# Kernel tuning notes

Hardware: AMD Instinct MI355X
Metric: run time of the kernel (lower is better)

## Reference

```python
import jax, jax.numpy as jnp
import numpy as np

B_SZ, D, HW, STRIDE, HEADS, DK, DV = 32, 64, 64, 4, 2, 32, 32
N = HW * HW                      # 4096 query tokens
M = (HW // STRIDE) ** 2          # 256 key/value tokens
EPS = 1e-5


def setup_inputs() -> dict:
    key = jax.random.key(0)
    ks = jax.random.split(key, 8)
    w = lambda k, s: jax.random.normal(k, s, dtype=jnp.float32) * 0.02
    return {
        "x": jax.random.normal(ks[0], (B_SZ, D, HW, HW), dtype=jnp.float32),
        "W_dw": jax.random.normal(ks[1], (D, 1, STRIDE, STRIDE), dtype=jnp.float32) * 0.1,
        "b_dw": jnp.zeros((D,), jnp.float32),
        "Wq": w(ks[2], (HEADS * DK, D)), "bq": jnp.zeros((HEADS * DK,), jnp.float32),
        "Wk": w(ks[3], (HEADS * DK, D)), "bk": jnp.zeros((HEADS * DK,), jnp.float32),
        "Wv": w(ks[4], (HEADS * DV, D)), "bv": jnp.zeros((HEADS * DV,), jnp.float32),
        "Wo": w(ks[5], (D, HEADS * DV)), "bo": jnp.zeros((D,), jnp.float32),
        "B": jax.random.normal(ks[6], (1, HEADS, N, M), dtype=jnp.float32),
    }


def reference(x, W_dw, b_dw, Wq, bq, Wk, bk, Wv, bv, Wo, bo, B):
    b, c, h, w = x.shape
    heads = B.shape[1]
    dk = Wq.shape[0] // heads
    dv = Wv.shape[0] // heads
    s = W_dw.shape[-1]

    # LayerNorm over (C, H, W), no affine params
    mu = jnp.mean(x, axis=(1, 2, 3), keepdims=True)
    var = jnp.mean((x - mu) ** 2, axis=(1, 2, 3), keepdims=True)
    xn = (x - mu) * jax.lax.rsqrt(var + EPS)

    # Q from normalized input: (b, N, c)
    xr = jnp.transpose(xn.reshape(b, c, h * w), (0, 2, 1))
    q = (xr @ Wq.T + bq).reshape(b, h * w, heads, dk).transpose(0, 2, 1, 3)

    # K/V from depthwise-conv downsample of the *unnormalized* x (as in source)
    kc = jax.lax.conv_general_dilated(
        x, W_dw, window_strides=(s, s), padding="VALID",
        feature_group_count=c,
        dimension_numbers=("NCHW", "OIHW", "NCHW"),
    ) + b_dw[None, :, None, None]
    kh, kw = kc.shape[2], kc.shape[3]
    kv_in = jnp.transpose(kc.reshape(b, c, kh * kw), (0, 2, 1))  # (b, M, c)
    k = (kv_in @ Wk.T + bk).reshape(b, kh * kw, heads, dk).transpose(0, 2, 1, 3)
    v = (kv_in @ Wv.T + bv).reshape(b, kh * kw, heads, dv).transpose(0, 2, 1, 3)

    # Attention with additive relative bias
    attn = jnp.einsum("bhid,bhjd->bhij", q, k) * (dk ** -0.5) + B
    attn = jax.nn.softmax(attn, axis=-1)
    tmp = jnp.einsum("bhij,bhjd->bhid", attn, v)           # (b, heads, N, dv)
    tmp = tmp.transpose(0, 2, 1, 3).reshape(b, h * w, heads * dv)

    # Output proj; NOTE: source does a raw .view(b, d, h, w) (reshape, not permute)
    out = (tmp @ Wo.T + bo).reshape(b, c, h, w)
    return out + x
```

## Files before the change

### kernel.cpp

```cpp
#include <hip/hip_runtime.h>

typedef float f32x4 __attribute__((ext_vector_type(4)));

#define MFMA8(a, b, c) __builtin_amdgcn_mfma_f32_16x16x32_fp8_fp8((long)(a), (long)(b), (c), 0, 0, 0)

__device__ __forceinline__ unsigned char f2fp8(float v) {
    int pk = __builtin_amdgcn_cvt_pk_fp8_f32(v, v, 0, false);
    return (unsigned char)(pk & 0xff);
}
__device__ __forceinline__ long packrow8(const float* p) {
    f32x4 a = *(const f32x4*)(p);
    f32x4 b = *(const f32x4*)(p + 4);
    int lo = __builtin_amdgcn_cvt_pk_fp8_f32(a.x, a.y, 0, false);
    lo = __builtin_amdgcn_cvt_pk_fp8_f32(a.z, a.w, lo, true);
    int hi = __builtin_amdgcn_cvt_pk_fp8_f32(b.x, b.y, 0, false);
    hi = __builtin_amdgcn_cvt_pk_fp8_f32(b.z, b.w, hi, true);
    return (long)(((unsigned long)(unsigned int)hi << 32) | (unsigned int)lo);
}
__device__ __forceinline__ int pack4(const float* p) {
    int v = __builtin_amdgcn_cvt_pk_fp8_f32(p[0], p[1], 0, false);
    return __builtin_amdgcn_cvt_pk_fp8_f32(p[2], p[3], v, true);
}

__global__ __launch_bounds__(256) void k_ln_part(const float* __restrict__ x,
                                                 float* __restrict__ part) {
    const int chunk = blockIdx.x, b = blockIdx.y, t = threadIdx.x;
    const float4* p = (const float4*)(x + b * 262144 + chunk * 16384);
    float s = 0.f, ss = 0.f;
    #pragma unroll
    for (int r = 0; r < 16; ++r) {
        float4 v = p[r * 256 + t];
        s  += v.x + v.y + v.z + v.w;
        ss += v.x * v.x + v.y * v.y + v.z * v.z + v.w * v.w;
    }
    #pragma unroll
    for (int off = 32; off > 0; off >>= 1) {
        s  += __shfl_down(s, off);
        ss += __shfl_down(ss, off);
    }
    __shared__ float sm[8];
    int wv = t >> 6;
    if ((t & 63) == 0) { sm[wv * 2] = s; sm[wv * 2 + 1] = ss; }
    __syncthreads();
    if (t == 0) {
        float S  = sm[0] + sm[2] + sm[4] + sm[6];
        float SS = sm[1] + sm[3] + sm[5] + sm[7];
        part[(b * 16 + chunk) * 2]     = S;
        part[(b * 16 + chunk) * 2 + 1] = SS;
    }
}

__global__ void k_ln_fin(const float* __restrict__ part, float* __restrict__ stats) {
    int t = threadIdx.x;
    if (t < 32) {
        float S = 0.f, SS = 0.f;
        for (int k = 0; k < 16; ++k) {
            S  += part[(t * 16 + k) * 2];
            SS += part[(t * 16 + k) * 2 + 1];
        }
        const float inv = 1.0f / 262144.0f;
        float mu  = S * inv;
        float var = SS * inv - mu * mu;
        stats[t * 2]     = mu;
        stats[t * 2 + 1] = rsqrtf(var + 1e-5f);
    }
}

__global__ __launch_bounds__(512) void k_kvb2(
    const float* __restrict__ x, const float* __restrict__ Wdw, const float* __restrict__ bdw,
    const float* __restrict__ Wk, const float* __restrict__ bk,
    const float* __restrict__ Wv, const float* __restrict__ bv,
    unsigned char* __restrict__ Kg, unsigned char* __restrict__ Vg,
    float* __restrict__ part)
{
    __shared__ __align__(16) unsigned char Y[16 * 72];
    __shared__ float sm[16];
    const int mi = blockIdx.x, b = blockIdx.y;
    const int t = threadIdx.x, w = t >> 6, lane = t & 63;
    const int quad = lane >> 4, l = lane & 15;
    const float* xb = x + b * 262144;

    const int s2l = lane & 3, mjl = lane >> 2;
    float s = 0.f, ss = 0.f;
    #pragma unroll
    for (int ci = 0; ci < 8; ++ci) {
        int c = w * 8 + ci;
        float wd0 = Wdw[c * 16 + 0 + s2l];
        float wd1 = Wdw[c * 16 + 4 + s2l];
        float wd2 = Wdw[c * 16 + 8 + s2l];
        float wd3 = Wdw[c * 16 + 12 + s2l];
        const float* xr = xb + c * 4096 + mi * 256;
        float v0 = xr[lane], v1 = xr[64 + lane], v2 = xr[128 + lane], v3 = xr[192 + lane];
        s  += v0 + v1 + v2 + v3;
        ss += v0 * v0 + v1 * v1 + v2 * v2 + v3 * v3;
        float acc = v0 * wd0;
        acc = fmaf(v1, wd1, acc);
        acc = fmaf(v2, wd2, acc);
        acc = fmaf(v3, wd3, acc);
        acc += __shfl_xor(acc, 1);
        acc += __shfl_xor(acc, 2);
        if (s2l == 0) Y[mjl * 72 + c] = f2fp8(acc + bdw[c]);
    }
    #pragma unroll
    for (int off = 32; off > 0; off >>= 1) {
        s  += __shfl_down(s, off);
        ss += __shfl_down(ss, off);
    }
    if (lane == 0) { sm[w * 2] = s; sm[w * 2 + 1] = ss; }
    __syncthreads();
    if (t == 0) {
        float S = 0.f, SS = 0.f;
        #pragma unroll
        for (int i = 0; i < 8; ++i) { S += sm[i * 2]; SS += sm[i * 2 + 1]; }
        part[(b * 16 + mi) * 2]     = S;
        part[(b * 16 + mi) * 2 + 1] = SS;
    }

    long ya0 = *(const long*)(Y + l * 72 + quad * 8);
    long ya1 = *(const long*)(Y + l * 72 + 32 + quad * 8);
    if (w < 4) {
        int e4 = w;
        long f0 = packrow8(Wk + (e4 * 16 + l) * 64 + quad * 8);
        long f1 = packrow8(Wk + (e4 * 16 + l) * 64 + 32 + quad * 8);
        float bb = bk[e4 * 16 + l];
        f32x4 c = { bb, bb, bb, bb };
        c = MFMA8(ya0, f0, c);
        c = MFMA8(ya1, f1, c);
        unsigned char* kd = Kg + b * 16384 + (mi * 16 + quad * 4) * 64 + e4 * 16 + l;
        #pragma unroll
        for (int r = 0; r < 4; ++r) kd[r * 64] = f2fp8(c[r]);
    } else {
        int d4 = w - 4;
        long f0 = packrow8(Wv + (d4 * 16 + l) * 64 + quad * 8);
        long f1 = packrow8(Wv + (d4 * 16 + l) * 64 + 32 + quad * 8);
        f32x4 c = { bv[d4 * 16 + quad * 4 + 0], bv[d4 * 16 + quad * 4 + 1],
                    bv[d4 * 16 + quad * 4 + 2], bv[d4 * 16 + quad * 4 + 3] };
        c = MFMA8(f0, ya0, c);
        c = MFMA8(f1, ya1, c);
        unsigned char* vd = Vg + b * 16384 + (d4 * 16 + quad * 4) * 256 + mi * 16 + l;
        #pragma unroll
        for (int r = 0; r < 4; ++r) vd[r * 256] = f2fp8(c[r]);
    }
}

__global__ void k_prep(const float* __restrict__ part, const float* __restrict__ Wq,
                       const float* __restrict__ Wo, float* __restrict__ stats,
                       unsigned char* __restrict__ Wq8, unsigned char* __restrict__ Wo8)
{
    int t = threadIdx.x;
    if (t < 32) {
        float S = 0.f, SS = 0.f;
        for (int k = 0; k < 16; ++k) {
            S  += part[(t * 16 + k) * 2];
            SS += part[(t * 16 + k) * 2 + 1];
        }
        const float inv = 1.0f / 262144.0f;
        float mu  = S * inv;
        float var = SS * inv - mu * mu;
        stats[t * 2]     = mu;
        stats[t * 2 + 1] = rsqrtf(var + 1e-5f);
    }
    {
        float f[16];
        #pragma unroll
        for (int g = 0; g < 4; ++g) *(f32x4*)&f[g * 4] = *(const f32x4*)(Wq + t * 16 + g * 4);
        uint4 o;
        o.x = pack4(&f[0]); o.y = pack4(&f[4]); o.z = pack4(&f[8]); o.w = pack4(&f[12]);
        *(uint4*)(Wq8 + t * 16) = o;
    }
    {
        float f[16];
        #pragma unroll
        for (int g = 0; g < 4; ++g) *(f32x4*)&f[g * 4] = *(const f32x4*)(Wo + t * 16 + g * 4);
        uint4 o;
        o.x = pack4(&f[0]); o.y = pack4(&f[4]); o.z = pack4(&f[8]); o.w = pack4(&f[12]);
        *(uint4*)(Wo8 + t * 16) = o;
    }
}

__global__ __launch_bounds__(512, 6) void k_attn3(
    const float* __restrict__ x, const unsigned char* __restrict__ Wq8,
    const float* __restrict__ bq, const unsigned char* __restrict__ Wo8,
    const float* __restrict__ bo, const float* __restrict__ Bb,
    const float* __restrict__ stats, const unsigned char* __restrict__ Kg,
    const unsigned char* __restrict__ Vg, float* __restrict__ outp)
{
    __shared__ __align__(16) long smem8[6528];
    unsigned char* S = (unsigned char*)smem8;
    unsigned char* Kf = S;
    unsigned char* Vt = S + 20480;
    unsigned char* XS = S + 37888;
    unsigned char* QF = S + 42496;
    unsigned char* TS = S + 37888;
    const int tile = blockIdx.x, b = blockIdx.y;
    const int t = threadIdx.x, w = t >> 6, lane = t & 63;
    const int quad = lane >> 4, l = lane & 15;
    unsigned char* PS = S + 47104 + w * 640;
    const int n0 = tile * 64;
    const float mu = stats[2 * b], rstd = stats[2 * b + 1];
    const float* xb = x + b * 262144;
    const float SCALE = 0.17677669529663687f;

    const unsigned char* Kgb = Kg + b * 16384;
    const unsigned char* Vgb = Vg + b * 16384;
    #pragma unroll
    for (int r = 0; r < 2; ++r) {
        int idx = t + 512 * r;
        int m = idx >> 2, c16 = (idx & 3) * 16;
        *(uint4*)(Kf + m * 80 + c16) = *(const uint4*)(Kgb + m * 64 + c16);
        int d = idx >> 4, e16 = (idx & 15) * 16;
        *(uint4*)(Vt + d * 272 + e16) = *(const uint4*)(Vgb + d * 256 + e16);
    }
    #pragma unroll
    for (int ci = 0; ci < 8; ++ci) {
        int c = w * 8 + ci;
        float v = (xb[c * 4096 + n0 + lane] - mu) * rstd;
        XS[lane * 72 + c] = f2fp8(v);
    }
    const int rtq = w >> 1, ct0 = (w & 1) * 2;
    long wqF[4], woF[4];
    float bqr[2], bor[2];
    #pragma unroll
    for (int i = 0; i < 2; ++i) {
        #pragma unroll
        for (int st = 0; st < 2; ++st) {
            wqF[i * 2 + st] = *(const long*)(Wq8 + ((ct0 + i) * 16 + l) * 64 + st * 32 + quad * 8);
            woF[i * 2 + st] = *(const long*)(Wo8 + ((ct0 + i) * 16 + l) * 64 + st * 32 + quad * 8);
        }
        bqr[i] = bq[(ct0 + i) * 16 + l];
        bor[i] = bo[(ct0 + i) * 16 + l];
    }
    __syncthreads();

    {
        long xa0 = *(const long*)(XS + (rtq * 16 + l) * 72 + quad * 8);
        long xa1 = *(const long*)(XS + (rtq * 16 + l) * 72 + 32 + quad * 8);
        #pragma unroll
        for (int i = 0; i < 2; ++i) {
            f32x4 c = { bqr[i], bqr[i], bqr[i], bqr[i] };
            c = MFMA8(xa0, wqF[i * 2 + 0], c);
            c = MFMA8(xa1, wqF[i * 2 + 1], c);
            unsigned char* qd = QF + (rtq * 16 + quad * 4) * 72 + (ct0 + i) * 16 + l;
            #pragma unroll
            for (int r = 0; r < 4; ++r) qd[r * 72] = f2fp8(c[r]);
        }
    }
    __syncthreads();

    const int h = w & 1, nq = w >> 1;
    long qa = *(const long*)(QF + (nq * 16 + l) * 72 + h * 32 + quad * 8);
    f32x4 O0 = { 0, 0, 0, 0 }, O1 = { 0, 0, 0, 0 };
    float Lp[4] = { 0, 0, 0, 0 };
    const float* Bbase = Bb + h * 1048576 + (n0 + nq * 16 + quad * 4) * 256;

    float Bv[2][4];
    #pragma unroll
    for (int sub = 0; sub < 2; ++sub)
        #pragma unroll
        for (int r = 0; r < 4; ++r)
            Bv[sub][r] = Bbase[r * 256 + sub * 16 + l];

    #pragma unroll 2
    for (int mc = 0; mc < 8; ++mc) {
        float Bn[2][4];
        if (mc < 7) {
            #pragma unroll
            for (int sub = 0; sub < 2; ++sub)
                #pragma unroll
                for (int r = 0; r < 4; ++r)
                    Bn[sub][r] = Bbase[r * 256 + (mc * 2 + 2 + sub) * 16 + l];
        }
        long kb0 = *(const long*)(Kf + ((mc * 2 + 0) * 16 + l) * 80 + h * 32 + quad * 8);
        long kb1 = *(const long*)(Kf + ((mc * 2 + 1) * 16 + l) * 80 + h * 32 + quad * 8);
        #pragma unroll
        for (int sub = 0; sub < 2; ++sub) {
            f32x4 sc = { 0, 0, 0, 0 };
            sc = MFMA8(qa, sub ? kb1 : kb0, sc);
            unsigned char* pw = PS + (quad * 4) * 40 + sub * 16 + l;
            #pragma unroll
            for (int r = 0; r < 4; ++r) {
                float p = __expf(fmaf(sc[r], SCALE, Bv[sub][r]));
                Lp[r] += p;
                pw[r * 40] = f2fp8(p);
            }
        }
        long pa  = *(const long*)(PS + l * 40 + quad * 8);
        long vb0 = *(const long*)(Vt + (h * 32 + l) * 272 + mc * 32 + quad * 8);
        long vb1 = *(const long*)(Vt + (h * 32 + 16 + l) * 272 + mc * 32 + quad * 8);
        O0 = MFMA8(pa, vb0, O0);
        O1 = MFMA8(pa, vb1, O1);
        #pragma unroll
        for (int sub = 0; sub < 2; ++sub)
            #pragma unroll
            for (int r = 0; r < 4; ++r)
                Bv[sub][r] = Bn[sub][r];
    }
    #pragma unroll
    for (int r = 0; r < 4; ++r) {
        #pragma unroll
        for (int d = 1; d < 16; d <<= 1) Lp[r] += __shfl_xor(Lp[r], d);
    }
    {
        unsigned char* td = TS + (nq * 16 + quad * 4) * 72 + h * 32 + l;
        #pragma unroll
        for (int r = 0; r < 4; ++r) {
            float inv = 1.0f / Lp[r];
            td[r * 72]      = f2fp8(O0[r] * inv);
            td[r * 72 + 16] = f2fp8(O1[r] * inv);
        }
    }
    __syncthreads();

    {
        long ta0 = *(const long*)(TS + (rtq * 16 + l) * 72 + quad * 8);
        long ta1 = *(const long*)(TS + (rtq * 16 + l) * 72 + 32 + quad * 8);
        float* ob = outp + b * 262144 + tile * 4096;
        const float* xr2 = xb + tile * 4096;
        #pragma unroll
        for (int i = 0; i < 2; ++i) {
            f32x4 c = { bor[i], bor[i], bor[i], bor[i] };
            c = MFMA8(ta0, woF[i * 2 + 0], c);
            c = MFMA8(ta1, woF[i * 2 + 1], c);
            #pragma unroll
            for (int r = 0; r < 4; ++r) {
                int off = (rtq * 16 + quad * 4 + r) * 64 + (ct0 + i) * 16 + l;
                ob[off] = c[r] + xr2[off];
            }
        }
    }
}

__global__ __launch_bounds__(512) void k_fused(
    const float* __restrict__ x, const float* __restrict__ Wdw, const float* __restrict__ bdw,
    const float* __restrict__ Wq, const float* __restrict__ bq,
    const float* __restrict__ Wk, const float* __restrict__ bk,
    const float* __restrict__ Wv, const float* __restrict__ bv,
    const float* __restrict__ Wo, const float* __restrict__ bo,
    const float* __restrict__ Bb, const float* __restrict__ stats,
    float* __restrict__ outp)
{
    __shared__ long smem8[6784];
    unsigned char* S = (unsigned char*)smem8;
    unsigned char* Kf = S;
    unsigned char* Vt = S + 18432;
    unsigned char* Y  = S + 35328;
    unsigned char* XS = S + 35328;
    unsigned char* QF = S + 35328 + 4608;
    unsigned char* TS = S + 35328 + 14336;

    const int tg = blockIdx.x, b = blockIdx.y;
    const int t = threadIdx.x, w = t >> 6, lane = t & 63;
    const int quad = lane >> 4, l = lane & 15;
    unsigned char* PS = S + 35328 + 9216 + w * 640;

    const float mu = stats[2 * b], rstd = stats[2 * b + 1];
    const float* xb = x + b * 262144;
    const float SCALE = 0.17677669529663687f;

    long wkF[8], wvF[8];
    #pragma unroll
    for (int e4 = 0; e4 < 4; ++e4)
        #pragma unroll
        for (int st = 0; st < 2; ++st) {
            wkF[e4 * 2 + st] = packrow8(Wk + (e4 * 16 + l) * 64 + st * 32 + quad * 8);
            wvF[e4 * 2 + st] = packrow8(Wv + (e4 * 16 + l) * 64 + st * 32 + quad * 8);
        }
    const int rtq = w >> 1, ct0 = (w & 1) * 2;
    long wqF[4], woF[4];
    #pragma unroll
    for (int i = 0; i < 2; ++i)
        #pragma unroll
        for (int st = 0; st < 2; ++st) {
            wqF[i * 2 + st] = packrow8(Wq + ((ct0 + i) * 16 + l) * 64 + st * 32 + quad * 8);
            woF[i * 2 + st] = packrow8(Wo + ((ct0 + i) * 16 + l) * 64 + st * 32 + quad * 8);
        }
    float bkr[4], bvr[4][4], bqr[2], bor[2];
    #pragma unroll
    for (int e4 = 0; e4 < 4; ++e4) bkr[e4] = bk[e4 * 16 + l];
    #pragma unroll
    for (int d4 = 0; d4 < 4; ++d4)
        #pragma unroll
        for (int r = 0; r < 4; ++r) bvr[d4][r] = bv[d4 * 16 + quad * 4 + r];
    #pragma unroll
    for (int i = 0; i < 2; ++i) { bqr[i] = bq[(ct0 + i) * 16 + l]; bor[i] = bo[(ct0 + i) * 16 + l]; }

    {
        const int s2l = lane & 3, mjl = lane >> 2;
        for (int ci = 0; ci < 8; ++ci) {
            int c = w * 8 + ci;
            float wd0 = Wdw[c * 16 + 0 + s2l];
            float wd1 = Wdw[c * 16 + 4 + s2l];
            float wd2 = Wdw[c * 16 + 8 + s2l];
            float wd3 = Wdw[c * 16 + 12 + s2l];
            float bdc = bdw[c];
            #pragma unroll 4
            for (int mi = 0; mi < 16; ++mi) {
                const float* xr = xb + c * 4096 + mi * 256;
                float acc = xr[lane] * wd0;
                acc = fmaf(xr[64 + lane],  wd1, acc);
                acc = fmaf(xr[128 + lane], wd2, acc);
                acc = fmaf(xr[192 + lane], wd3, acc);
                acc += __shfl_xor(acc, 1);
                acc += __shfl_xor(acc, 2);
                if (s2l == 0) Y[(mi * 16 + mjl) * 72 + c] = f2fp8(acc + bdc);
            }
        }
    }
    __syncthreads();

    #pragma unroll
    for (int i = 0; i < 2; ++i) {
        int rt = w * 2 + i;
        long ya0 = *(const long*)(Y + (rt * 16 + l) * 72 + quad * 8);
        long ya1 = *(const long*)(Y + (rt * 16 + l) * 72 + 32 + quad * 8);
        #pragma unroll
        for (int e4 = 0; e4 < 4; ++e4) {
            f32x4 c = { bkr[e4], bkr[e4], bkr[e4], bkr[e4] };
            c = MFMA8(ya0, wkF[e4 * 2 + 0], c);
            c = MFMA8(ya1, wkF[e4 * 2 + 1], c);
            unsigned char* kd = Kf + (rt * 16 + quad * 4) * 72 + e4 * 16 + l;
            #pragma unroll
            for (int r = 0; r < 4; ++r) kd[r * 72] = f2fp8(c[r]);
        }
        #pragma unroll
        for (int d4 = 0; d4 < 4; ++d4) {
            f32x4 c = { bvr[d4][0], bvr[d4][1], bvr[d4][2], bvr[d4][3] };
            c = MFMA8(wvF[d4 * 2 + 0], ya0, c);
            c = MFMA8(wvF[d4 * 2 + 1], ya1, c);
            unsigned char* vd = Vt + (d4 * 16 + quad * 4) * 264 + rt * 16 + l;
            #pragma unroll
            for (int r = 0; r < 4; ++r) vd[r * 264] = f2fp8(c[r]);
        }
    }
    __syncthreads();

    const int h = w & 1, nq = w >> 1;

    for (int tile = 0; tile < 8; ++tile) {
        const int tidx = tg * 8 + tile, n0 = tidx * 64;

        for (int ci = 0; ci < 8; ++ci) {
            int c = w * 8 + ci;
            float v = (xb[c * 4096 + n0 + lane] - mu) * rstd;
            XS[lane * 72 + c] = f2fp8(v);
        }
        __syncthreads();

        {
            long xa0 = *(const long*)(XS + (rtq * 16 + l) * 72 + quad * 8);
            long xa1 = *(const long*)(XS + (rtq * 16 + l) * 72 + 32 + quad * 8);
            #pragma unroll
            for (int i = 0; i < 2; ++i) {
                f32x4 c = { bqr[i], bqr[i], bqr[i], bqr[i] };
                c = MFMA8(xa0, wqF[i * 2 + 0], c);
                c = MFMA8(xa1, wqF[i * 2 + 1], c);
                unsigned char* qd = QF + (rtq * 16 + quad * 4) * 72 + (ct0 + i) * 16 + l;
                #pragma unroll
                for (int r = 0; r < 4; ++r) qd[r * 72] = f2fp8(c[r]);
            }
        }
        __syncthreads();

        long qa = *(const long*)(QF + (nq * 16 + l) * 72 + h * 32 + quad * 8);
        f32x4 O0 = { 0, 0, 0, 0 }, O1 = { 0, 0, 0, 0 };
        float Lp[4] = { 0, 0, 0, 0 };
        const float* Bbase = Bb + h * 1048576 + (n0 + nq * 16 + quad * 4) * 256;

        #pragma unroll 2
        for (int mc = 0; mc < 8; ++mc) {
            #pragma unroll
            for (int sub = 0; sub < 2; ++sub) {
                int mt = mc * 2 + sub;
                long kb = *(const long*)(Kf + (mt * 16 + l) * 72 + h * 32 + quad * 8);
                f32x4 sc = { 0, 0, 0, 0 };
                sc = MFMA8(qa, kb, sc);
                unsigned char* pw = PS + (quad * 4) * 40 + sub * 16 + l;
                #pragma unroll
                for (int r = 0; r < 4; ++r) {
                    float p = __expf(fmaf(sc[r], SCALE, Bbase[r * 256 + mt * 16 + l]));
                    Lp[r] += p;
                    pw[r * 40] = f2fp8(p);
                }
            }
            long pa  = *(const long*)(PS + l * 40 + quad * 8);
            long vb0 = *(const long*)(Vt + (h * 32 + l) * 264 + mc * 32 + quad * 8);
            long vb1 = *(const long*)(Vt + (h * 32 + 16 + l) * 264 + mc * 32 + quad * 8);
            O0 = MFMA8(pa, vb0, O0);
            O1 = MFMA8(pa, vb1, O1);
        }
        #pragma unroll
        for (int r = 0; r < 4; ++r) {
            #pragma unroll
            for (int d = 1; d < 16; d <<= 1) Lp[r] += __shfl_xor(Lp[r], d);
        }
        {
            unsigned char* td = TS + (nq * 16 + quad * 4) * 72 + h * 32 + l;
            #pragma unroll
            for (int r = 0; r < 4; ++r) {
                float inv = 1.0f / Lp[r];
                td[r * 72]      = f2fp8(O0[r] * inv);
                td[r * 72 + 16] = f2fp8(O1[r] * inv);
            }
        }
        __syncthreads();

        {
            long ta0 = *(const long*)(TS + (rtq * 16 + l) * 72 + quad * 8);
            long ta1 = *(const long*)(TS + (rtq * 16 + l) * 72 + 32 + quad * 8);
            float* ob = outp + b * 262144 + tidx * 4096;
            const float* xr2 = xb + tidx * 4096;
            #pragma unroll
            for (int i = 0; i < 2; ++i) {
                f32x4 c = { bor[i], bor[i], bor[i], bor[i] };
                c = MFMA8(ta0, woF[i * 2 + 0], c);
                c = MFMA8(ta1, woF[i * 2 + 1], c);
                #pragma unroll
                for (int r = 0; r < 4; ++r) {
                    int off = (rtq * 16 + quad * 4 + r) * 64 + (ct0 + i) * 16 + l;
                    ob[off] = c[r] + xr2[off];
                }
            }
        }
        __syncthreads();
    }
}

extern "C" void kernel_launch(void* const* d_in, const int* in_sizes, int n_in,
                              void* d_out, int out_size, void* d_ws, size_t ws_size,
                              hipStream_t stream) {
    (void)in_sizes; (void)n_in; (void)out_size;
    const float* x   = (const float*)d_in[0];
    const float* Wdw = (const float*)d_in[1];
    const float* bdw = (const float*)d_in[2];
    const float* Wq  = (const float*)d_in[3];
    const float* bq  = (const float*)d_in[4];
    const float* Wk  = (const float*)d_in[5];
    const float* bk  = (const float*)d_in[6];
    const float* Wv  = (const float*)d_in[7];
    const float* bv  = (const float*)d_in[8];
    const float* Wo  = (const float*)d_in[9];
    const float* bo  = (const float*)d_in[10];
    const float* Bb  = (const float*)d_in[11];
    float* outp = (float*)d_out;

    float* ws    = (float*)d_ws;
    float* part  = ws;
    float* stats = ws + 1024;
    unsigned char* Wq8 = (unsigned char*)d_ws + 8192;
    unsigned char* Wo8 = (unsigned char*)d_ws + 12288;
    unsigned char* Kg  = (unsigned char*)d_ws + 16384;
    unsigned char* Vg  = Kg + 524288;

    if (ws_size >= (size_t)(16384 + 2 * 524288)) {
        k_kvb2<<<dim3(16, 32), 512, 0, stream>>>(x, Wdw, bdw, Wk, bk, Wv, bv, Kg, Vg, part);
        k_prep<<<1, 256, 0, stream>>>(part, Wq, Wo, stats, Wq8, Wo8);
        k_attn3<<<dim3(64, 32), 512, 0, stream>>>(x, Wq8, bq, Wo8, bo, Bb, stats, Kg, Vg, outp);
    } else {
        k_ln_part<<<dim3(16, 32), 256, 0, stream>>>(x, part);
        k_ln_fin<<<1, 64, 0, stream>>>(part, stats);
        k_fused<<<dim3(8, 32), 512, 0, stream>>>(x, Wdw, bdw, Wq, bq, Wk, bk, Wv, bv,
                                                 Wo, bo, Bb, stats, outp);
    }
}
```

Baseline: 149.0 us.

## Remove prep kernel, fold weight packing and LN stats; keep P in registers

Drops the single-block k_prep launch. Its Wq/Wo fp8 packing moves into block (0,0) of k_kvb2, and every attention block now reduces the LayerNorm partial sums itself. The attention inner loop computes the transposed score MFMA (K as A operand) so the bias is read as contiguous float4 rows. The P operand for the PV MFMA is rebuilt with cross-lane shuffles instead of a round trip through LDS. This removes a launch and the LDS staging of P and reduces LDS footprint, at the cost of redundant per-block stats reduction and extra shuffles.

After: 157.1 us. 1.05x slower.

```diff
diff --git a/kernel.cpp b/kernel.cpp
--- a/kernel.cpp
+++ b/kernel.cpp
@@ -70,8 +70,9 @@
     const float* __restrict__ x, const float* __restrict__ Wdw, const float* __restrict__ bdw,
     const float* __restrict__ Wk, const float* __restrict__ bk,
     const float* __restrict__ Wv, const float* __restrict__ bv,
+    const float* __restrict__ Wq, const float* __restrict__ Wo,
     unsigned char* __restrict__ Kg, unsigned char* __restrict__ Vg,
-    float* __restrict__ part)
+    float* __restrict__ part, unsigned char* __restrict__ Wq8, unsigned char* __restrict__ Wo8)
 {
     __shared__ __align__(16) unsigned char Y[16 * 72];
     __shared__ float sm[16];
@@ -79,6 +80,19 @@
     const int t = threadIdx.x, w = t >> 6, lane = t & 63;
     const int quad = lane >> 4, l = lane & 15;
     const float* xb = x + b * 262144;
+
+    if ((mi | b) == 0) {
+        float f[8];
+        #pragma unroll
+        for (int g = 0; g < 2; ++g) *(f32x4*)&f[g * 4] = *(const f32x4*)(Wq + t * 8 + g * 4);
+        int2 o;
+        o.x = pack4(f); o.y = pack4(f + 4);
+        *(int2*)(Wq8 + t * 8) = o;
+        #pragma unroll
+        for (int g = 0; g < 2; ++g) *(f32x4*)&f[g * 4] = *(const f32x4*)(Wo + t * 8 + g * 4);
+        o.x = pack4(f); o.y = pack4(f + 4);
+        *(int2*)(Wo8 + t * 8) = o;
+    }
 
     const int s2l = lane & 3, mjl = lane >> 2;
     float s = 0.f, ss = 0.f;
@@ -143,49 +157,14 @@
     }
 }
 
-__global__ void k_prep(const float* __restrict__ part, const float* __restrict__ Wq,
-                       const float* __restrict__ Wo, float* __restrict__ stats,
-                       unsigned char* __restrict__ Wq8, unsigned char* __restrict__ Wo8)
-{
-    int t = threadIdx.x;
-    if (t < 32) {
-        float S = 0.f, SS = 0.f;
-        for (int k = 0; k < 16; ++k) {
-            S  += part[(t * 16 + k) * 2];
-            SS += part[(t * 16 + k) * 2 + 1];
-        }
-        const float inv = 1.0f / 262144.0f;
-        float mu  = S * inv;
-        float var = SS * inv - mu * mu;
-        stats[t * 2]     = mu;
-        stats[t * 2 + 1] = rsqrtf(var + 1e-5f);
-    }
-    {
-        float f[16];
-        #pragma unroll
-        for (int g = 0; g < 4; ++g) *(f32x4*)&f[g * 4] = *(const f32x4*)(Wq + t * 16 + g * 4);
-        uint4 o;
-        o.x = pack4(&f[0]); o.y = pack4(&f[4]); o.z = pack4(&f[8]); o.w = pack4(&f[12]);
-        *(uint4*)(Wq8 + t * 16) = o;
-    }
-    {
-        float f[16];
-        #pragma unroll
-        for (int g = 0; g < 4; ++g) *(f32x4*)&f[g * 4] = *(const f32x4*)(Wo + t * 16 + g * 4);
-        uint4 o;
-        o.x = pack4(&f[0]); o.y = pack4(&f[4]); o.z = pack4(&f[8]); o.w = pack4(&f[12]);
-        *(uint4*)(Wo8 + t * 16) = o;
-    }
-}
-
 __global__ __launch_bounds__(512, 6) void k_attn3(
     const float* __restrict__ x, const unsigned char* __restrict__ Wq8,
     const float* __restrict__ bq, const unsigned char* __restrict__ Wo8,
     const float* __restrict__ bo, const float* __restrict__ Bb,
-    const float* __restrict__ stats, const unsigned char* __restrict__ Kg,
+    const float* __restrict__ part, const unsigned char* __restrict__ Kg,
     const unsigned char* __restrict__ Vg, float* __restrict__ outp)
 {
-    __shared__ __align__(16) long smem8[6528];
+    __shared__ __align__(16) long smem8[5888];
     unsigned char* S = (unsigned char*)smem8;
     unsigned char* Kf = S;
     unsigned char* Vt = S + 20480;
@@ -195,11 +174,19 @@
     const int tile = blockIdx.x, b = blockIdx.y;
     const int t = threadIdx.x, w = t >> 6, lane = t & 63;
     const int quad = lane >> 4, l = lane & 15;
-    unsigned char* PS = S + 47104 + w * 640;
     const int n0 = tile * 64;
-    const float mu = stats[2 * b], rstd = stats[2 * b + 1];
     const float* xb = x + b * 262144;
     const float SCALE = 0.17677669529663687f;
+
+    float Sp = 0.f, SSp = 0.f;
+    #pragma unroll
+    for (int k2 = 0; k2 < 16; ++k2) {
+        Sp  += part[(b * 16 + k2) * 2];
+        SSp += part[(b * 16 + k2) * 2 + 1];
+    }
+    const float invN = 1.0f / 262144.0f;
+    const float mu = Sp * invN;
+    const float rstd = rsqrtf(SSp * invN - mu * mu + 1e-5f);
 
     const unsigned char* Kgb = Kg + b * 16384;
     const unsigned char* Vgb = Vg + b * 16384;
@@ -250,63 +237,69 @@
     const int h = w & 1, nq = w >> 1;
     long qa = *(const long*)(QF + (nq * 16 + l) * 72 + h * 32 + quad * 8);
     f32x4 O0 = { 0, 0, 0, 0 }, O1 = { 0, 0, 0, 0 };
-    float Lp[4] = { 0, 0, 0, 0 };
-    const float* Bbase = Bb + h * 1048576 + (n0 + nq * 16 + quad * 4) * 256;
-
-    float Bv[2][4];
-    #pragma unroll
-    for (int sub = 0; sub < 2; ++sub)
-        #pragma unroll
-        for (int r = 0; r < 4; ++r)
-            Bv[sub][r] = Bbase[r * 256 + sub * 16 + l];
+    float Lsum = 0.f;
+    const float* Brow = Bb + h * 1048576 + (n0 + nq * 16 + l) * 256 + quad * 4;
+
+    f32x4 Bv0 = *(const f32x4*)(Brow);
+    f32x4 Bv1 = *(const f32x4*)(Brow + 16);
 
     #pragma unroll 2
     for (int mc = 0; mc < 8; ++mc) {
-        float Bn[2][4];
+        f32x4 Bn0, Bn1;
         if (mc < 7) {
-            #pragma unroll
-            for (int sub = 0; sub < 2; ++sub)
-                #pragma unroll
-                for (int r = 0; r < 4; ++r)
-                    Bn[sub][r] = Bbase[r * 256 + (mc * 2 + 2 + sub) * 16 + l];
+            Bn0 = *(const f32x4*)(Brow + (mc * 2 + 2) * 16);
+            Bn1 = *(const f32x4*)(Brow + (mc * 2 + 3) * 16);
         }
         long kb0 = *(const long*)(Kf + ((mc * 2 + 0) * 16 + l) * 80 + h * 32 + quad * 8);
         long kb1 = *(const long*)(Kf + ((mc * 2 + 1) * 16 + l) * 80 + h * 32 + quad * 8);
-        #pragma unroll
-        for (int sub = 0; sub < 2; ++sub) {
+        int pk0, pk1;
+        {
             f32x4 sc = { 0, 0, 0, 0 };
-            sc = MFMA8(qa, sub ? kb1 : kb0, sc);
-            unsigned char* pw = PS + (quad * 4) * 40 + sub * 16 + l;
+            sc = MFMA8(kb0, qa, sc);
+            float pf[4];
             #pragma unroll
             for (int r = 0; r < 4; ++r) {
-                float p = __expf(fmaf(sc[r], SCALE, Bv[sub][r]));
-                Lp[r] += p;
-                pw[r * 40] = f2fp8(p);
-            }
-        }
-        long pa  = *(const long*)(PS + l * 40 + quad * 8);
+                float p = __expf(fmaf(sc[r], SCALE, Bv0[r]));
+                Lsum += p;
+                pf[r] = p;
+            }
+            pk0 = pack4(pf);
+        }
+        {
+            f32x4 sc = { 0, 0, 0, 0 };
+            sc = MFMA8(kb1, qa, sc);
+            float pf[4];
+            #pragma unroll
+            for (int r = 0; r < 4; ++r) {
+                float p = __expf(fmaf(sc[r], SCALE, Bv1[r]));
+                Lsum += p;
+                pf[r] = p;
+            }
+            pk1 = pack4(pf);
+        }
+        int sel = (quad < 2) ? pk0 : pk1;
+        int srcl = l + ((quad & 1) << 5);
+        int lo = __shfl(sel, srcl);
+        int hi = __shfl(sel, srcl + 16);
+        long pa = (long)(((unsigned long)(unsigned int)hi << 32) | (unsigned int)lo);
         long vb0 = *(const long*)(Vt + (h * 32 + l) * 272 + mc * 32 + quad * 8);
         long vb1 = *(const long*)(Vt + (h * 32 + 16 + l) * 272 + mc * 32 + quad * 8);
         O0 = MFMA8(pa, vb0, O0);
         O1 = MFMA8(pa, vb1, O1);
-        #pragma unroll
-        for (int sub = 0; sub < 2; ++sub)
-            #pragma unroll
-            for (int r = 0; r < 4; ++r)
-                Bv[sub][r] = Bn[sub][r];
-    }
-    #pragma unroll
-    for (int r = 0; r < 4; ++r) {
-        #pragma unroll
-        for (int d = 1; d < 16; d <<= 1) Lp[r] += __shfl_xor(Lp[r], d);
-    }
+        Bv0 = Bn0; Bv1 = Bn1;
+    }
+    Lsum += __shfl_xor(Lsum, 16);
+    Lsum += __shfl_xor(Lsum, 32);
+    float inv = 1.0f / Lsum;
+    float invr[4];
+    #pragma unroll
+    for (int r = 0; r < 4; ++r) invr[r] = __shfl(inv, quad * 4 + r);
     {
         unsigned char* td = TS + (nq * 16 + quad * 4) * 72 + h * 32 + l;
         #pragma unroll
         for (int r = 0; r < 4; ++r) {
-            float inv = 1.0f / Lp[r];
-            td[r * 72]      = f2fp8(O0[r] * inv);
-            td[r * 72 + 16] = f2fp8(O1[r] * inv);
+            td[r * 72]      = f2fp8(O0[r] * invr[r]);
+            td[r * 72 + 16] = f2fp8(O1[r] * invr[r]);
         }
     }
     __syncthreads();
@@ -552,9 +545,9 @@
     unsigned char* Vg  = Kg + 524288;
 
     if (ws_size >= (size_t)(16384 + 2 * 524288)) {
-        k_kvb2<<<dim3(16, 32), 512, 0, stream>>>(x, Wdw, bdw, Wk, bk, Wv, bv, Kg, Vg, part);
-        k_prep<<<1, 256, 0, stream>>>(part, Wq, Wo, stats, Wq8, Wo8);
-        k_attn3<<<dim3(64, 32), 512, 0, stream>>>(x, Wq8, bq, Wo8, bo, Bb, stats, Kg, Vg, outp);
+        k_kvb2<<<dim3(16, 32), 512, 0, stream>>>(x, Wdw, bdw, Wk, bk, Wv, bv, Wq, Wo,
+                                                 Kg, Vg, part, Wq8, Wo8);
+        k_attn3<<<dim3(64, 32), 512, 0, stream>>>(x, Wq8, bq, Wo8, bo, Bb, part, Kg, Vg, outp);
     } else {
         k_ln_part<<<dim3(16, 32), 256, 0, stream>>>(x, part);
         k_ln_fin<<<1, 64, 0, stream>>>(part, stats);
```

## Fold prep kernel into KV and attention kernels; process two tiles per block

Applied to the files above, without the earlier changes.

Removes the single-block k_prep launch. Its weight fp8 conversion moves into block (0,0) of the KV kernel, and the LayerNorm statistics are recomputed from the partial sums at the start of each attention block. The attention kernel now handles two 64-token tiles per block, which halves the grid and amortises the K/V shared-memory staging and weight fragment loads. The cost is less parallelism per launch, an added barrier per tile, and redundant statistic reductions in every block.

Result: slower. 170.7 us (+14.5%).

```diff
diff --git a/kernel.cpp b/kernel.cpp
--- a/kernel.cpp
+++ b/kernel.cpp
@@ -70,8 +70,9 @@
     const float* __restrict__ x, const float* __restrict__ Wdw, const float* __restrict__ bdw,
     const float* __restrict__ Wk, const float* __restrict__ bk,
     const float* __restrict__ Wv, const float* __restrict__ bv,
+    const float* __restrict__ Wq, const float* __restrict__ Wo,
     unsigned char* __restrict__ Kg, unsigned char* __restrict__ Vg,
-    float* __restrict__ part)
+    float* __restrict__ part, unsigned char* __restrict__ Wq8, unsigned char* __restrict__ Wo8)
 {
     __shared__ __align__(16) unsigned char Y[16 * 72];
     __shared__ float sm[16];
@@ -79,6 +80,19 @@
     const int t = threadIdx.x, w = t >> 6, lane = t & 63;
     const int quad = lane >> 4, l = lane & 15;
     const float* xb = x + b * 262144;
+
+    if ((mi | b) == 0) {
+        float f[8];
+        #pragma unroll
+        for (int g = 0; g < 2; ++g) *(f32x4*)&f[g * 4] = *(const f32x4*)(Wq + t * 8 + g * 4);
+        int2 o;
+        o.x = pack4(f); o.y = pack4(f + 4);
+        *(int2*)(Wq8 + t * 8) = o;
+        #pragma unroll
+        for (int g = 0; g < 2; ++g) *(f32x4*)&f[g * 4] = *(const f32x4*)(Wo + t * 8 + g * 4);
+        o.x = pack4(f); o.y = pack4(f + 4);
+        *(int2*)(Wo8 + t * 8) = o;
+    }
 
     const int s2l = lane & 3, mjl = lane >> 2;
     float s = 0.f, ss = 0.f;
@@ -143,46 +157,11 @@
     }
 }
 
-__global__ void k_prep(const float* __restrict__ part, const float* __restrict__ Wq,
-                       const float* __restrict__ Wo, float* __restrict__ stats,
-                       unsigned char* __restrict__ Wq8, unsigned char* __restrict__ Wo8)
-{
-    int t = threadIdx.x;
-    if (t < 32) {
-        float S = 0.f, SS = 0.f;
-        for (int k = 0; k < 16; ++k) {
-            S  += part[(t * 16 + k) * 2];
-            SS += part[(t * 16 + k) * 2 + 1];
-        }
-        const float inv = 1.0f / 262144.0f;
-        float mu  = S * inv;
-        float var = SS * inv - mu * mu;
-        stats[t * 2]     = mu;
-        stats[t * 2 + 1] = rsqrtf(var + 1e-5f);
-    }
-    {
-        float f[16];
-        #pragma unroll
-        for (int g = 0; g < 4; ++g) *(f32x4*)&f[g * 4] = *(const f32x4*)(Wq + t * 16 + g * 4);
-        uint4 o;
-        o.x = pack4(&f[0]); o.y = pack4(&f[4]); o.z = pack4(&f[8]); o.w = pack4(&f[12]);
-        *(uint4*)(Wq8 + t * 16) = o;
-    }
-    {
-        float f[16];
-        #pragma unroll
-        for (int g = 0; g < 4; ++g) *(f32x4*)&f[g * 4] = *(const f32x4*)(Wo + t * 16 + g * 4);
-        uint4 o;
-        o.x = pack4(&f[0]); o.y = pack4(&f[4]); o.z = pack4(&f[8]); o.w = pack4(&f[12]);
-        *(uint4*)(Wo8 + t * 16) = o;
-    }
-}
-
-__global__ __launch_bounds__(512, 6) void k_attn3(
+__global__ __launch_bounds__(512, 6) void k_attn4(
     const float* __restrict__ x, const unsigned char* __restrict__ Wq8,
     const float* __restrict__ bq, const unsigned char* __restrict__ Wo8,
     const float* __restrict__ bo, const float* __restrict__ Bb,
-    const float* __restrict__ stats, const unsigned char* __restrict__ Kg,
+    const float* __restrict__ part, const unsigned char* __restrict__ Kg,
     const unsigned char* __restrict__ Vg, float* __restrict__ outp)
 {
     __shared__ __align__(16) long smem8[6528];
@@ -192,14 +171,22 @@
     unsigned char* XS = S + 37888;
     unsigned char* QF = S + 42496;
     unsigned char* TS = S + 37888;
-    const int tile = blockIdx.x, b = blockIdx.y;
+    const int b = blockIdx.y;
     const int t = threadIdx.x, w = t >> 6, lane = t & 63;
     const int quad = lane >> 4, l = lane & 15;
     unsigned char* PS = S + 47104 + w * 640;
-    const int n0 = tile * 64;
-    const float mu = stats[2 * b], rstd = stats[2 * b + 1];
     const float* xb = x + b * 262144;
     const float SCALE = 0.17677669529663687f;
+
+    float Sp = 0.f, SSp = 0.f;
+    #pragma unroll
+    for (int k2 = 0; k2 < 16; ++k2) {
+        Sp  += part[(b * 16 + k2) * 2];
+        SSp += part[(b * 16 + k2) * 2 + 1];
+    }
+    const float invN = 1.0f / 262144.0f;
+    const float mu = Sp * invN;
+    const float rstd = rsqrtf(SSp * invN - mu * mu + 1e-5f);
 
     const unsigned char* Kgb = Kg + b * 16384;
     const unsigned char* Vgb = Vg + b * 16384;
@@ -211,12 +198,6 @@
         int d = idx >> 4, e16 = (idx & 15) * 16;
         *(uint4*)(Vt + d * 272 + e16) = *(const uint4*)(Vgb + d * 256 + e16);
     }
-    #pragma unroll
-    for (int ci = 0; ci < 8; ++ci) {
-        int c = w * 8 + ci;
-        float v = (xb[c * 4096 + n0 + lane] - mu) * rstd;
-        XS[lane * 72 + c] = f2fp8(v);
-    }
     const int rtq = w >> 1, ct0 = (w & 1) * 2;
     long wqF[4], woF[4];
     float bqr[2], bor[2];
@@ -230,103 +211,114 @@
         bqr[i] = bq[(ct0 + i) * 16 + l];
         bor[i] = bo[(ct0 + i) * 16 + l];
     }
-    __syncthreads();
-
-    {
-        long xa0 = *(const long*)(XS + (rtq * 16 + l) * 72 + quad * 8);
-        long xa1 = *(const long*)(XS + (rtq * 16 + l) * 72 + 32 + quad * 8);
-        #pragma unroll
-        for (int i = 0; i < 2; ++i) {
-            f32x4 c = { bqr[i], bqr[i], bqr[i], bqr[i] };
-            c = MFMA8(xa0, wqF[i * 2 + 0], c);
-            c = MFMA8(xa1, wqF[i * 2 + 1], c);
-            unsigned char* qd = QF + (rtq * 16 + quad * 4) * 72 + (ct0 + i) * 16 + l;
-            #pragma unroll
-            for (int r = 0; r < 4; ++r) qd[r * 72] = f2fp8(c[r]);
-        }
-    }
-    __syncthreads();
-
     const int h = w & 1, nq = w >> 1;
-    long qa = *(const long*)(QF + (nq * 16 + l) * 72 + h * 32 + quad * 8);
-    f32x4 O0 = { 0, 0, 0, 0 }, O1 = { 0, 0, 0, 0 };
-    float Lp[4] = { 0, 0, 0, 0 };
-    const float* Bbase = Bb + h * 1048576 + (n0 + nq * 16 + quad * 4) * 256;
-
-    float Bv[2][4];
-    #pragma unroll
-    for (int sub = 0; sub < 2; ++sub)
-        #pragma unroll
-        for (int r = 0; r < 4; ++r)
-            Bv[sub][r] = Bbase[r * 256 + sub * 16 + l];
-
-    #pragma unroll 2
-    for (int mc = 0; mc < 8; ++mc) {
-        float Bn[2][4];
-        if (mc < 7) {
+
+    for (int tl = 0; tl < 2; ++tl) {
+        const int tile = blockIdx.x * 2 + tl, n0 = tile * 64;
+
+        #pragma unroll
+        for (int ci = 0; ci < 8; ++ci) {
+            int c = w * 8 + ci;
+            float v = (xb[c * 4096 + n0 + lane] - mu) * rstd;
+            XS[lane * 72 + c] = f2fp8(v);
+        }
+        const float* Bbase = Bb + h * 1048576 + (n0 + nq * 16 + quad * 4) * 256;
+        float Bv[2][4];
+        #pragma unroll
+        for (int sub = 0; sub < 2; ++sub)
+            #pragma unroll
+            for (int r = 0; r < 4; ++r)
+                Bv[sub][r] = Bbase[r * 256 + sub * 16 + l];
+        __syncthreads();
+
+        {
+            long xa0 = *(const long*)(XS + (rtq * 16 + l) * 72 + quad * 8);
+            long xa1 = *(const long*)(XS + (rtq * 16 + l) * 72 + 32 + quad * 8);
+            #pragma unroll
+            for (int i = 0; i < 2; ++i) {
+                f32x4 c = { bqr[i], bqr[i], bqr[i], bqr[i] };
+                c = MFMA8(xa0, wqF[i * 2 + 0], c);
+                c = MFMA8(xa1, wqF[i * 2 + 1], c);
+                unsigned char* qd = QF + (rtq * 16 + quad * 4) * 72 + (ct0 + i) * 16 + l;
+                #pragma unroll
+                for (int r = 0; r < 4; ++r) qd[r * 72] = f2fp8(c[r]);
+            }
+        }
+        __syncthreads();
+
+        long qa = *(const long*)(QF + (nq * 16 + l) * 72 + h * 32 + quad * 8);
+        f32x4 O0 = { 0, 0, 0, 0 }, O1 = { 0, 0, 0, 0 };
+        float Lp[4] = { 0, 0, 0, 0 };
+
+        #pragma unroll 2
+        for (int mc = 0; mc < 8; ++mc) {
+            float Bn[2][4];
+            if (mc < 7) {
+                #pragma unroll
+                for (int sub = 0; sub < 2; ++sub)
+                    #pragma unroll
+                    for (int r = 0; r < 4; ++r)
+                        Bn[sub][r] = Bbase[r * 256 + (mc * 2 + 2 + sub) * 16 + l];
+            }
+            long kb0 = *(const long*)(Kf + ((mc * 2 + 0) * 16 + l) * 80 + h * 32 + quad * 8);
+            long kb1 = *(const long*)(Kf + ((mc * 2 + 1) * 16 + l) * 80 + h * 32 + quad * 8);
+            #pragma unroll
+            for (int sub = 0; sub < 2; ++sub) {
+                f32x4 sc = { 0, 0, 0, 0 };
+                sc = MFMA8(qa, sub ? kb1 : kb0, sc);
+                unsigned char* pw = PS + (quad * 4) * 40 + sub * 16 + l;
+                #pragma unroll
+                for (int r = 0; r < 4; ++r) {
+                    float p = __expf(fmaf(sc[r], SCALE, Bv[sub][r]));
+                    Lp[r] += p;
+                    pw[r * 40] = f2fp8(p);
+                }
+            }
+            long pa  = *(const long*)(PS + l * 40 + quad * 8);
+            long vb0 = *(const long*)(Vt + (h * 32 + l) * 272 + mc * 32 + quad * 8);
+            long vb1 = *(const long*)(Vt + (h * 32 + 16 + l) * 272 + mc * 32 + quad * 8);
+            O0 = MFMA8(pa, vb0, O0);
+            O1 = MFMA8(pa, vb1, O1);
             #pragma unroll
             for (int sub = 0; sub < 2; ++sub)
                 #pragma unroll
                 for (int r = 0; r < 4; ++r)
-                    Bn[sub][r] = Bbase[r * 256 + (mc * 2 + 2 + sub) * 16 + l];
-        }
-        long kb0 = *(const long*)(Kf + ((mc * 2 + 0) * 16 + l) * 80 + h * 32 + quad * 8);
-        long kb1 = *(const long*)(Kf + ((mc * 2 + 1) * 16 + l) * 80 + h * 32 + quad * 8);
-        #pragma unroll
-        for (int sub = 0; sub < 2; ++sub) {
-            f32x4 sc = { 0, 0, 0, 0 };
-            sc = MFMA8(qa, sub ? kb1 : kb0, sc);
-            unsigned char* pw = PS + (quad * 4) * 40 + sub * 16 + l;
+                    Bv[sub][r] = Bn[sub][r];
+        }
+        #pragma unroll
+        for (int r = 0; r < 4; ++r) {
+            #pragma unroll
+            for (int d = 1; d < 16; d <<= 1) Lp[r] += __shfl_xor(Lp[r], d);
+        }
+        {
+            unsigned char* td = TS + (nq * 16 + quad * 4) * 72 + h * 32 + l;
             #pragma unroll
             for (int r = 0; r < 4; ++r) {
-                float p = __expf(fmaf(sc[r], SCALE, Bv[sub][r]));
-                Lp[r] += p;
-                pw[r * 40] = f2fp8(p);
-            }
-        }
-        long pa  = *(const long*)(PS + l * 40 + quad * 8);
-        long vb0 = *(const long*)(Vt + (h * 32 + l) * 272 + mc * 32 + quad * 8);
-        long vb1 = *(const long*)(Vt + (h * 32 + 16 + l) * 272 + mc * 32 + quad * 8);
-        O0 = MFMA8(pa, vb0, O0);
-        O1 = MFMA8(pa, vb1, O1);
-        #pragma unroll
-        for (int sub = 0; sub < 2; ++sub)
-            #pragma unroll
-            for (int r = 0; r < 4; ++r)
-                Bv[sub][r] = Bn[sub][r];
-    }
-    #pragma unroll
-    for (int r = 0; r < 4; ++r) {
-        #pragma unroll
-        for (int d = 1; d < 16; d <<= 1) Lp[r] += __shfl_xor(Lp[r], d);
-    }
-    {
-        unsigned char* td = TS + (nq * 16 + quad * 4) * 72 + h * 32 + l;
-        #pragma unroll
-        for (int r = 0; r < 4; ++r) {
-            float inv = 1.0f / Lp[r];
-            td[r * 72]      = f2fp8(O0[r] * inv);
-            td[r * 72 + 16] = f2fp8(O1[r] * inv);
-        }
-    }
-    __syncthreads();
-
-    {
-        long ta0 = *(const long*)(TS + (rtq * 16 + l) * 72 + quad * 8);
-        long ta1 = *(const long*)(TS + (rtq * 16 + l) * 72 + 32 + quad * 8);
-        float* ob = outp + b * 262144 + tile * 4096;
-        const float* xr2 = xb + tile * 4096;
-        #pragma unroll
-        for (int i = 0; i < 2; ++i) {
-            f32x4 c = { bor[i], bor[i], bor[i], bor[i] };
-            c = MFMA8(ta0, woF[i * 2 + 0], c);
-            c = MFMA8(ta1, woF[i * 2 + 1], c);
-            #pragma unroll
-            for (int r = 0; r < 4; ++r) {
-                int off = (rtq * 16 + quad * 4 + r) * 64 + (ct0 + i) * 16 + l;
-                ob[off] = c[r] + xr2[off];
-            }
-        }
+                float inv = 1.0f / Lp[r];
+                td[r * 72]      = f2fp8(O0[r] * inv);
+                td[r * 72 + 16] = f2fp8(O1[r] * inv);
+            }
+        }
+        __syncthreads();
+
+        {
+            long ta0 = *(const long*)(TS + (rtq * 16 + l) * 72 + quad * 8);
+            long ta1 = *(const long*)(TS + (rtq * 16 + l) * 72 + 32 + quad * 8);
+            float* ob = outp + b * 262144 + tile * 4096;
+            const float* xr2 = xb + tile * 4096;
+            #pragma unroll
+            for (int i = 0; i < 2; ++i) {
+                f32x4 c = { bor[i], bor[i], bor[i], bor[i] };
+                c = MFMA8(ta0, woF[i * 2 + 0], c);
+                c = MFMA8(ta1, woF[i * 2 + 1], c);
+                #pragma unroll
+                for (int r = 0; r < 4; ++r) {
+                    int off = (rtq * 16 + quad * 4 + r) * 64 + (ct0 + i) * 16 + l;
+                    ob[off] = c[r] + xr2[off];
+                }
+            }
+        }
+        __syncthreads();
     }
 }
 
@@ -552,9 +544,9 @@
     unsigned char* Vg  = Kg + 524288;
 
     if (ws_size >= (size_t)(16384 + 2 * 524288)) {
-        k_kvb2<<<dim3(16, 32), 512, 0, stream>>>(x, Wdw, bdw, Wk, bk, Wv, bv, Kg, Vg, part);
-        k_prep<<<1, 256, 0, stream>>>(part, Wq, Wo, stats, Wq8, Wo8);
-        k_attn3<<<dim3(64, 32), 512, 0, stream>>>(x, Wq8, bq, Wo8, bo, Bb, stats, Kg, Vg, outp);
+        k_kvb2<<<dim3(16, 32), 512, 0, stream>>>(x, Wdw, bdw, Wk, bk, Wv, bv, Wq, Wo,
+                                                 Kg, Vg, part, Wq8, Wo8);
+        k_attn4<<<dim3(32, 32), 512, 0, stream>>>(x, Wq8, bq, Wo8, bo, Bb, part, Kg, Vg, outp);
     } else {
         k_ln_part<<<dim3(16, 32), 256, 0, stream>>>(x, part);
         k_ln_fin<<<1, 64, 0, stream>>>(part, stats);
```
